# Performance work log

Hardware: AMD Instinct MI355X
Metric: run time of the kernel (lower is better)

## Reference

```python
import jax, jax.numpy as jnp
import numpy as np

EPS_BN = 1e-5


def _square_distance(a, b):
    # a: [B,N,3], b: [B,S,3] -> [B,N,S]
    return (jnp.sum(a * a, -1)[:, :, None]
            - 2.0 * jnp.einsum('bnc,bsc->bns', a, b)
            + jnp.sum(b * b, -1)[:, None, :])


def _bn_relu(x, gamma, beta):
    # x: [B,C,N]; training-mode batch norm over (B,N) per channel
    mean = jnp.mean(x, axis=(0, 2), keepdims=True)
    var = jnp.var(x, axis=(0, 2), keepdims=True)
    y = (x - mean) * jax.lax.rsqrt(var + EPS_BN)
    y = y * gamma[None, :, None] + beta[None, :, None]
    return jax.nn.relu(y)


def setup_inputs() -> dict:
    key = jax.random.key(0)
    ks = jax.random.split(key, 8)
    B, N, S, D1, D2 = 16, 4096, 1024, 128, 256
    Cin, C0, C1 = D1 + D2, 256, 128
    inp = {
        'xyz1': jax.random.normal(ks[0], (B, 3, N), jnp.float32),
        'xyz2': jax.random.normal(ks[1], (B, 3, S), jnp.float32),
        'points1': jax.random.normal(ks[2], (B, D1, N), jnp.float32),
        'points2': jax.random.normal(ks[3], (B, D2, S), jnp.float32),
        # pointwise Conv1d weights (kernel size 1) as [out,in]
        'w0': jax.random.normal(ks[4], (C0, Cin), jnp.float32) * (1.0 / np.sqrt(Cin)),
        'b0': jnp.zeros((C0,), jnp.float32),
        'g0': jnp.ones((C0,), jnp.float32),
        'be0': jnp.zeros((C0,), jnp.float32),
        'w1': jax.random.normal(ks[5], (C1, C0), jnp.float32) * (1.0 / np.sqrt(C0)),
        'b1': jnp.zeros((C1,), jnp.float32),
        'g1': jnp.ones((C1,), jnp.float32),
        'be1': jnp.zeros((C1,), jnp.float32),
    }
    return inp


def reference(xyz1, xyz2, points1, points2, w0, b0, g0, be0, w1, b1, g1, be1):
    # permute to [B,N,3] / [B,S,3] / [B,S,D2]
    x1 = jnp.transpose(xyz1, (0, 2, 1))
    x2 = jnp.transpose(xyz2, (0, 2, 1))
    p2 = jnp.transpose(points2, (0, 2, 1))
    B, N, _ = x1.shape

    dists = _square_distance(x1, x2)            # [B,N,S]
    # NOTE: faithful to the source: idx comes from the sort, but the
    # weight distances are the FIRST 3 columns of the UNsorted dists
    # (the repo assigns sorted values to `dicts`, not `dists`).
    idx = jnp.argsort(dists, axis=-1)[:, :, :3]  # [B,N,3]
    d3 = jnp.maximum(dists[:, :, :3], 1e-10)     # [B,N,3]
    weight = 1.0 / d3
    weight = weight / jnp.sum(weight, axis=-1, keepdims=True)

    gathered = jax.vmap(lambda p, i: p[i])(p2, idx)          # [B,N,3,D2]
    interpolated = jnp.sum(gathered * weight[..., None], axis=2)  # [B,N,D2]

    p1 = jnp.transpose(points1, (0, 2, 1))       # [B,N,D1]
    new_points = jnp.concatenate([p1, interpolated], axis=-1)  # [B,N,Cin]
    new_points = jnp.transpose(new_points, (0, 2, 1))           # [B,Cin,N]

    h = jnp.einsum('oc,bcn->bon', w0, new_points) + b0[None, :, None]
    h = _bn_relu(h, g0, be0)
    h = jnp.einsum('oc,bcn->bon', w1, h) + b1[None, :, None]
    h = _bn_relu(h, g1, be1)
    return h
```

## Files before the change

### kernel.cpp

```cpp
#include <hip/hip_runtime.h>
#include <cstdint>
#include <cstddef>

#define BB   16
#define NN   4096
#define SS   1024
#define D1   128
#define D2   256
#define CIN  384
#define C0   256
#define C1   128
#define MM   (BB*NN)
#define NBLK (MM/128)

typedef __attribute__((ext_vector_type(8))) short short8;
typedef __attribute__((ext_vector_type(4))) float f32x4;

__device__ __forceinline__ float b2f(unsigned short h) {
    union { unsigned int u; float f; } x; x.u = ((unsigned int)h) << 16; return x.f;
}
__device__ __forceinline__ unsigned short f2b(float f) {
    union { float f; unsigned int u; } x; x.f = f;
    unsigned int r = x.u + 0x7FFFu + ((x.u >> 16) & 1u);
    return (unsigned short)(r >> 16);
}

#define GLD16(g, l) __builtin_amdgcn_global_load_lds( \
    (const __attribute__((address_space(1))) void*)(g), \
    (__attribute__((address_space(3))) void*)(l), 16, 0, 0)

__global__ void transpose_cast_k(const float* __restrict__ src, unsigned short* __restrict__ dst,
                                 int C, int Np, int dstStride)
{
    __shared__ float tile[64][65];
    const int b = blockIdx.z, c0 = blockIdx.y * 64, n0 = blockIdx.x * 64;
    const int t = threadIdx.x, j = t & 63, i4 = t >> 6;
#pragma unroll
    for (int p = 0; p < 64; p += 4) {
        int ci = p + i4;
        tile[ci][j] = src[((size_t)b * C + c0 + ci) * Np + n0 + j];
    }
    __syncthreads();
#pragma unroll
    for (int p = 0; p < 64; p += 4) {
        int ni = p + i4;
        dst[((size_t)b * Np + n0 + ni) * dstStride + c0 + j] = f2b(tile[j][ni]);
    }
}

__global__ void cvtw_k(const float* __restrict__ w0, const float* __restrict__ w1,
                       unsigned short* __restrict__ w0b, unsigned short* __restrict__ w1b)
{
    int i = blockIdx.x * 256 + threadIdx.x;
    if (i < C0 * CIN) w0b[i] = f2b(w0[i]);
    if (i < C1 * C0)  w1b[i] = f2b(w1[i]);
}

#define UPD6(dd, ss, D0, D1v, D2v, J0, J1, J2) do { \
    bool ca = (dd) < D0, cb = (dd) < D1v, cc = (dd) < D2v; \
    float m1 = __builtin_amdgcn_fmed3f((dd), D0, D1v); \
    float m2 = __builtin_amdgcn_fmed3f((dd), D1v, D2v); \
    int u1 = ca ? J0 : (ss); \
    int u2 = cb ? J1 : (ss); \
    D0 = fminf((dd), D0); \
    J2 = cc ? u2 : J2; \
    J1 = cb ? u1 : J1; \
    J0 = ca ? (ss) : J0; \
    D1v = m1; D2v = m2; \
} while (0)

#define LTE(x, xj, y, yj) ((x) < (y) || ((x) == (y) && (xj) < (yj)))

__global__ __launch_bounds__(256) void knn_k(const float* __restrict__ xyz1,
                                             const float* __restrict__ xyz2,
                                             int* __restrict__ idxb, float* __restrict__ wtb)
{
    __shared__ __align__(16) float sx[8 * 132];
    __shared__ __align__(16) float sy[8 * 132];
    __shared__ __align__(16) float sz[8 * 132];
    const int b = blockIdx.y;
    const int t = threadIdx.x;
    const int chunk = t & 7;
    const int n = blockIdx.x * 32 + (t >> 3);

    for (int i = t; i < SS; i += 256) {
        int li = (i >> 7) * 132 + (i & 127);
        sx[li] = xyz2[((size_t)b * 3 + 0) * SS + i];
        sy[li] = xyz2[((size_t)b * 3 + 1) * SS + i];
        sz[li] = xyz2[((size_t)b * 3 + 2) * SS + i];
    }
    __syncthreads();

    const float px = xyz1[((size_t)b * 3 + 0) * NN + n];
    const float py = xyz1[((size_t)b * 3 + 1) * NN + n];
    const float pz = xyz1[((size_t)b * 3 + 2) * NN + n];

    float aD0 = 3.4e38f, aD1 = 3.4e38f, aD2 = 3.4e38f;
    int   aJ0 = 0, aJ1 = 0, aJ2 = 0;
    float bD0 = 3.4e38f, bD1 = 3.4e38f, bD2 = 3.4e38f;
    int   bJ0 = 0, bJ1 = 0, bJ2 = 0;

    const float* cx = sx + chunk * 132;
    const float* cy = sy + chunk * 132;
    const float* cz = sz + chunk * 132;
    const int sbase = chunk * 128;
#pragma unroll 4
    for (int s4 = 0; s4 < 32; ++s4) {
        float4 xs = *(const float4*)(cx + s4 * 4);
        float4 ys = *(const float4*)(cy + s4 * 4);
        float4 zs = *(const float4*)(cz + s4 * 4);
        int s = sbase + s4 * 4;
        { float dx=px-xs.x, dy=py-ys.x, dz=pz-zs.x; float d=dx*dx+dy*dy+dz*dz; UPD6(d, s+0, aD0,aD1,aD2,aJ0,aJ1,aJ2); }
        { float dx=px-xs.y, dy=py-ys.y, dz=pz-zs.y; float d=dx*dx+dy*dy+dz*dz; UPD6(d, s+1, bD0,bD1,bD2,bJ0,bJ1,bJ2); }
        { float dx=px-xs.z, dy=py-ys.z, dz=pz-zs.z; float d=dx*dx+dy*dy+dz*dz; UPD6(d, s+2, aD0,aD1,aD2,aJ0,aJ1,aJ2); }
        { float dx=px-xs.w, dy=py-ys.w, dz=pz-zs.w; float d=dx*dx+dy*dy+dz*dz; UPD6(d, s+3, bD0,bD1,bD2,bJ0,bJ1,bJ2); }
    }

    float d0v, d1v, d2v; int j0, j1, j2;
    {
        bool c0 = LTE(aD0, aJ0, bD0, bJ0);
        d0v = c0 ? aD0 : bD0;  j0 = c0 ? aJ0 : bJ0;
        float na0 = c0 ? aD1 : aD0, na1 = c0 ? aD2 : aD1;
        int   nx0 = c0 ? aJ1 : aJ0, nx1 = c0 ? aJ2 : aJ1;
        float nb0 = c0 ? bD0 : bD1, nb1 = c0 ? bD1 : bD2;
        int   ny0 = c0 ? bJ0 : bJ1, ny1 = c0 ? bJ1 : bJ2;
        bool c1 = LTE(na0, nx0, nb0, ny0);
        d1v = c1 ? na0 : nb0;  j1 = c1 ? nx0 : ny0;
        float ma0 = c1 ? na1 : na0;  int mx0 = c1 ? nx1 : nx0;
        float mb0 = c1 ? nb0 : nb1;  int my0 = c1 ? ny0 : ny1;
        bool c2 = LTE(ma0, mx0, mb0, my0);
        d2v = c2 ? ma0 : mb0;  j2 = c2 ? mx0 : my0;
    }

#pragma unroll
    for (int r = 1; r <= 4; r <<= 1) {
        float e0 = __shfl_xor(d0v, r), e1 = __shfl_xor(d1v, r), e2 = __shfl_xor(d2v, r);
        int   k0 = __shfl_xor(j0, r),  k1 = __shfl_xor(j1, r),  k2 = __shfl_xor(j2, r);
        bool ownlow = ((t & r) == 0);
        float a0 = ownlow ? d0v : e0, a1 = ownlow ? d1v : e1, a2 = ownlow ? d2v : e2;
        int   x0 = ownlow ? j0 : k0,  x1 = ownlow ? j1 : k1,  x2 = ownlow ? j2 : k2;
        float b0 = ownlow ? e0 : d0v, b1 = ownlow ? e1 : d1v, b2 = ownlow ? e2 : d2v;
        int   y0 = ownlow ? k0 : j0,  y1 = ownlow ? k1 : j1,  y2 = ownlow ? k2 : j2;
        bool c0 = a0 <= b0;
        d0v = c0 ? a0 : b0;  j0 = c0 ? x0 : y0;
        float na0 = c0 ? a1 : a0, na1 = c0 ? a2 : a1;
        int   nx0 = c0 ? x1 : x0, nx1 = c0 ? x2 : x1;
        float nb0 = c0 ? b0 : b1, nb1 = c0 ? b1 : b2;
        int   ny0 = c0 ? y0 : y1, ny1 = c0 ? y1 : y2;
        bool c1 = na0 <= nb0;
        d1v = c1 ? na0 : nb0;  j1 = c1 ? nx0 : ny0;
        float ma0 = c1 ? na1 : na0;  int mx0 = c1 ? nx1 : nx0;
        float mb0 = c1 ? nb0 : nb1;  int my0 = c1 ? ny0 : ny1;
        bool c2 = ma0 <= mb0;
        d2v = c2 ? ma0 : mb0;  j2 = c2 ? mx0 : my0;
    }

    if (chunk == 0) {
        float dd[3];
#pragma unroll
        for (int k = 0; k < 3; ++k) {
            float dx = px - sx[k], dy = py - sy[k], dz = pz - sz[k];
            float d = dx*dx + dy*dy + dz*dz;
            dd[k] = fmaxf(d, 1e-10f);
        }
        float r0 = 1.f/dd[0], r1 = 1.f/dd[1], r2 = 1.f/dd[2];
        float inv = 1.f / (r0 + r1 + r2);
        size_t base = ((size_t)b * NN + n) * 3;
        idxb[base+0] = j0; idxb[base+1] = j1; idxb[base+2] = j2;
        wtb[base+0] = r0*inv; wtb[base+1] = r1*inv; wtb[base+2] = r2*inv;
    }
}

__launch_bounds__(512, 1)
__global__ void gemm1_k(const unsigned short* __restrict__ P1T,
                        const unsigned short* __restrict__ P2T,
                        const int* __restrict__ idxb, const float* __restrict__ wtb,
                        const unsigned short* __restrict__ w0b,
                        unsigned short* __restrict__ h1, float* __restrict__ part1)
{
    __shared__ unsigned short Als[128 * 64];
    __shared__ unsigned short Bls[256 * 64];
    __shared__ float lsum[2][256];
    __shared__ float lsq[2][256];

    const int t = threadIdx.x;
    const int wv = t >> 6, l = t & 63, g = l >> 4, lc = l & 15;
    const int wm = wv >> 2, wn = wv & 3;
    const int m0 = blockIdx.x * 128;
    const int b  = blockIdx.x >> 5;
    const int sub = t & 7;

    const int grow = t >> 2;
    const size_t gb = ((size_t)(m0 + grow)) * 3;
    const int gi0 = idxb[gb], gi1 = idxb[gb+1], gi2 = idxb[gb+2];
    const float gw0 = wtb[gb], gw1 = wtb[gb+1], gw2 = wtb[gb+2];
    const char* gp0 = (const char*)(P2T + ((size_t)b * SS + gi0) * D2) + (t & 3) * 32;
    const char* gp1 = (const char*)(P2T + ((size_t)b * SS + gi1) * D2) + (t & 3) * 32;
    const char* gp2 = (const char*)(P2T + ((size_t)b * SS + gi2) * D2) + (t & 3) * 32;
    char* gdst = (char*)Als + grow * 128;
    const int gsw = (grow & 7) << 4;

    f32x4 acc[4][4];
#pragma unroll
    for (int i = 0; i < 4; ++i)
#pragma unroll
        for (int j = 0; j < 4; ++j) acc[i][j] = (f32x4){0.f, 0.f, 0.f, 0.f};

    for (int ks = 0; ks < 6; ++ks) {
        const int k0 = ks * 64;
        __syncthreads();
        if (ks < 2) {
#pragma unroll
            for (int q = 0; q < 2; ++q) {
                int row = q * 64 + (t >> 3);
                int bco = (sub * 16) ^ ((row & 7) << 4);
                const char* src = (const char*)P1T + (((size_t)(m0 + row)) * D1 + k0) * 2 + bco;
                char* dst = (char*)Als + (q * 512 + wv * 64) * 16;
                GLD16(src, dst);
            }
        } else {
            const int cgB = (ks - 2) * 128;
#pragma unroll
            for (int h = 0; h < 2; ++h) {
                union { uint4 v; unsigned short s[8]; } a0, a1, a2, ov;
                a0.v = *(const uint4*)(gp0 + cgB + h * 16);
                a1.v = *(const uint4*)(gp1 + cgB + h * 16);
                a2.v = *(const uint4*)(gp2 + cgB + h * 16);
#pragma unroll
                for (int i = 0; i < 8; ++i)
                    ov.s[i] = f2b(gw0 * b2f(a0.s[i]) + gw1 * b2f(a1.s[i]) + gw2 * b2f(a2.s[i]));
                *(uint4*)(gdst + (((t & 3) * 32 + h * 16) ^ gsw)) = ov.v;
            }
        }
#pragma unroll
        for (int q = 0; q < 4; ++q) {
            int o = q * 64 + (t >> 3);
            int bco = (sub * 16) ^ ((o & 7) << 4);
            const char* src = (const char*)w0b + (((size_t)o) * CIN + k0) * 2 + bco;
            char* dst = (char*)Bls + (q * 512 + wv * 64) * 16;
            GLD16(src, dst);
        }
        __syncthreads();
#pragma unroll
        for (int kk = 0; kk < 2; ++kk) {
            short8 af[4], bfr[4];
#pragma unroll
            for (int fm = 0; fm < 4; ++fm) {
                int row = wm * 64 + fm * 16 + lc;
                int bcol = kk * 64 + g * 16;
                af[fm] = *(const short8*)((const char*)Als + row * 128 + (bcol ^ ((row & 7) << 4)));
            }
#pragma unroll
            for (int fn = 0; fn < 4; ++fn) {
                int o = wn * 64 + fn * 16 + lc;
                int bcol = kk * 64 + g * 16;
                bfr[fn] = *(const short8*)((const char*)Bls + o * 128 + (bcol ^ ((o & 7) << 4)));
            }
#pragma unroll
            for (int fm = 0; fm < 4; ++fm)
#pragma unroll
                for (int fn = 0; fn < 4; ++fn)
                    acc[fm][fn] = __builtin_amdgcn_mfma_f32_16x16x32_bf16(af[fm], bfr[fn], acc[fm][fn], 0, 0, 0);
        }
    }

    float s1[4] = {0,0,0,0}, s2v[4] = {0,0,0,0};
#pragma unroll
    for (int fm = 0; fm < 4; ++fm)
#pragma unroll
        for (int fn = 0; fn < 4; ++fn) {
            int row = m0 + wm * 64 + fm * 16 + g * 4;
            int col = wn * 64 + fn * 16 + lc;
#pragma unroll
            for (int j = 0; j < 4; ++j) {
                float v = acc[fm][fn][j];
                h1[((size_t)(row + j)) * C0 + col] = f2b(v);
                s1[fn] += v; s2v[fn] += v * v;
            }
        }
#pragma unroll
    for (int fn = 0; fn < 4; ++fn) {
        s1[fn] += __shfl_xor(s1[fn], 16); s1[fn] += __shfl_xor(s1[fn], 32);
        s2v[fn] += __shfl_xor(s2v[fn], 16); s2v[fn] += __shfl_xor(s2v[fn], 32);
    }
    if (l < 16) {
#pragma unroll
        for (int fn = 0; fn < 4; ++fn) {
            lsum[wm][wn * 64 + fn * 16 + l] = s1[fn];
            lsq[wm][wn * 64 + fn * 16 + l] = s2v[fn];
        }
    }
    __syncthreads();
    if (t < 256) {
        part1[(size_t)t * NBLK + blockIdx.x]        = lsum[0][t] + lsum[1][t];
        part1[(size_t)(C0 + t) * NBLK + blockIdx.x] = lsq[0][t] + lsq[1][t];
    }
}

__global__ void stats_k(const float* __restrict__ part, int nblk, int C,
                        const float* __restrict__ gam, const float* __restrict__ bet,
                        float* __restrict__ sc, float* __restrict__ sh)
{
    const int w = threadIdx.x >> 6, l = threadIdx.x & 63;
    const int o = blockIdx.x * 4 + w;
    if (o >= C) return;
    float s = 0.f, q = 0.f;
    for (int i = l; i < nblk; i += 64) {
        s += part[(size_t)o * nblk + i];
        q += part[(size_t)(C + o) * nblk + i];
    }
#pragma unroll
    for (int r = 32; r; r >>= 1) { s += __shfl_xor(s, r); q += __shfl_xor(q, r); }
    if (l == 0) {
        const float inv = 1.0f / (float)MM;
        float mean = s * inv;
        float var = q * inv - mean * mean;
        float scale = gam[o] * rsqrtf(var + 1e-5f);
        sc[o] = scale;
        sh[o] = bet[o] - mean * scale;
    }
}

__launch_bounds__(256, 1)
__global__ void gemm2_k(const unsigned short* __restrict__ h1, const unsigned short* __restrict__ w1b,
                        const float* __restrict__ sc1, const float* __restrict__ sh1,
                        unsigned short* __restrict__ h2, float* __restrict__ part2)
{
    __shared__ unsigned short Als[128 * 64];
    __shared__ unsigned short Bls[128 * 64];
    __shared__ float scl[256], shl[256];
    __shared__ float lsum[2][128];
    __shared__ float lsq[2][128];

    const int t = threadIdx.x;
    const int wv = t >> 6, l = t & 63, g = l >> 4, lc = l & 15;
    const int wm = wv >> 1, wn = wv & 1;
    const int m0 = blockIdx.x * 128;
    const int sub = t & 7;

    scl[t] = sc1[t]; shl[t] = sh1[t];

    f32x4 acc[4][4];
#pragma unroll
    for (int i = 0; i < 4; ++i)
#pragma unroll
        for (int j = 0; j < 4; ++j) acc[i][j] = (f32x4){0.f, 0.f, 0.f, 0.f};

    for (int ks = 0; ks < 4; ++ks) {
        const int k0 = ks * 64;
        __syncthreads();
        uint4 r[4];
#pragma unroll
        for (int q = 0; q < 4; ++q) {
            int row = q * 32 + (t >> 3);
            r[q] = *(const uint4*)((const char*)h1 + (((size_t)(m0 + row)) * C0 + k0) * 2 + sub * 16);
        }
#pragma unroll
        for (int q = 0; q < 4; ++q) {
            int row = q * 32 + (t >> 3);
            union { uint4 v; unsigned short s[8]; } u, ov;
            u.v = r[q];
#pragma unroll
            for (int i = 0; i < 8; ++i) {
                int k = k0 + sub * 8 + i;
                float f = b2f(u.s[i]);
                ov.s[i] = f2b(fmaxf(0.0f, fmaf(scl[k], f, shl[k])));
            }
            *(uint4*)((char*)Als + row * 128 + ((sub * 16) ^ ((row & 7) << 4))) = ov.v;
        }
#pragma unroll
        for (int q = 0; q < 4; ++q) {
            int o = q * 32 + (t >> 3);
            int bco = (sub * 16) ^ ((o & 7) << 4);
            const char* src = (const char*)w1b + (((size_t)o) * C0 + k0) * 2 + bco;
            char* dst = (char*)Bls + (q * 256 + wv * 64) * 16;
            GLD16(src, dst);
        }
        __syncthreads();
#pragma unroll
        for (int kk = 0; kk < 2; ++kk) {
            short8 af[4], bfr[4];
#pragma unroll
            for (int fm = 0; fm < 4; ++fm) {
                int row = wm * 64 + fm * 16 + lc;
                int bcol = kk * 64 + g * 16;
                af[fm] = *(const short8*)((const char*)Als + row * 128 + (bcol ^ ((row & 7) << 4)));
            }
#pragma unroll
            for (int fn = 0; fn < 4; ++fn) {
                int o = wn * 64 + fn * 16 + lc;
                int bcol = kk * 64 + g * 16;
                bfr[fn] = *(const short8*)((const char*)Bls + o * 128 + (bcol ^ ((o & 7) << 4)));
            }
#pragma unroll
            for (int fm = 0; fm < 4; ++fm)
#pragma unroll
                for (int fn = 0; fn < 4; ++fn)
                    acc[fm][fn] = __builtin_amdgcn_mfma_f32_16x16x32_bf16(af[fm], bfr[fn], acc[fm][fn], 0, 0, 0);
        }
    }

    float s1[4] = {0,0,0,0}, s2v[4] = {0,0,0,0};
#pragma unroll
    for (int fm = 0; fm < 4; ++fm)
#pragma unroll
        for (int fn = 0; fn < 4; ++fn) {
            int row = m0 + wm * 64 + fm * 16 + g * 4;
            int col = wn * 64 + fn * 16 + lc;
#pragma unroll
            for (int j = 0; j < 4; ++j) {
                float v = acc[fm][fn][j];
                h2[((size_t)(row + j)) * C1 + col] = f2b(v);
                s1[fn] += v; s2v[fn] += v * v;
            }
        }
#pragma unroll
    for (int fn = 0; fn < 4; ++fn) {
        s1[fn] += __shfl_xor(s1[fn], 16); s1[fn] += __shfl_xor(s1[fn], 32);
        s2v[fn] += __shfl_xor(s2v[fn], 16); s2v[fn] += __shfl_xor(s2v[fn], 32);
    }
    if (l < 16) {
#pragma unroll
        for (int fn = 0; fn < 4; ++fn) {
            lsum[wm][wn * 64 + fn * 16 + l] = s1[fn];
            lsq[wm][wn * 64 + fn * 16 + l] = s2v[fn];
        }
    }
    __syncthreads();
    if (t < 128) {
        part2[(size_t)t * NBLK + blockIdx.x]        = lsum[0][t] + lsum[1][t];
        part2[(size_t)(C1 + t) * NBLK + blockIdx.x] = lsq[0][t] + lsq[1][t];
    }
}

__global__ void finalize_k(const unsigned short* __restrict__ h2,
                           const float* __restrict__ sc, const float* __restrict__ sh,
                           float* __restrict__ out)
{
    __shared__ float tile[64][65];
    const int b = blockIdx.z, o0 = blockIdx.y * 64, n0 = blockIdx.x * 64;
    const int t = threadIdx.x, j = t & 63, i4 = t >> 6;
    const float scv = sc[o0 + j], shv = sh[o0 + j];
#pragma unroll
    for (int p = 0; p < 64; p += 4) {
        int ni = p + i4;
        float f = b2f(h2[((size_t)b * NN + n0 + ni) * C1 + o0 + j]);
        tile[ni][j] = fmaxf(0.0f, fmaf(scv, f, shv));
    }
    __syncthreads();
#pragma unroll
    for (int p = 0; p < 64; p += 4) {
        int oi = p + i4;
        out[((size_t)(b * C1 + o0 + oi)) * NN + n0 + j] = tile[j][oi];
    }
}

extern "C" void kernel_launch(void* const* d_in, const int* in_sizes, int n_in,
                              void* d_out, int out_size, void* d_ws, size_t ws_size,
                              hipStream_t stream)
{
    const float* xyz1    = (const float*)d_in[0];
    const float* xyz2    = (const float*)d_in[1];
    const float* points1 = (const float*)d_in[2];
    const float* points2 = (const float*)d_in[3];
    const float* w0      = (const float*)d_in[4];
    const float* g0      = (const float*)d_in[6];
    const float* be0     = (const float*)d_in[7];
    const float* w1      = (const float*)d_in[8];
    const float* g1      = (const float*)d_in[10];
    const float* be1     = (const float*)d_in[11];
    float* out = (float*)d_out;
    char* ws = (char*)d_ws;

    unsigned short* P1T = (unsigned short*)(ws + 0);
    unsigned short* h1  = (unsigned short*)(ws + 16777216);
    unsigned short* P2T = (unsigned short*)(ws + 50331648);
    unsigned short* h2  = (unsigned short*)(ws + 58720256);
    int*   idxb  = (int*)  (ws + 75497472);
    float* wtb   = (float*)(ws + 76283904);
    unsigned short* w0b = (unsigned short*)(ws + 77070336);
    unsigned short* w1b = (unsigned short*)(ws + 77266944);
    float* part1 = (float*)(ws + 77332480);
    float* part2 = (float*)(ws + 78381056);
    float* sc1   = (float*)(ws + 78905344);
    float* sh1   = (float*)(ws + 78906368);
    float* sc2   = (float*)(ws + 78907392);
    float* sh2   = (float*)(ws + 78908416);

    transpose_cast_k<<<dim3(NN/64, D1/64, BB), 256, 0, stream>>>(points1, P1T, D1, NN, D1);
    transpose_cast_k<<<dim3(SS/64, D2/64, BB), 256, 0, stream>>>(points2, P2T, D2, SS, D2);
    cvtw_k<<<(C0*CIN)/256, 256, 0, stream>>>(w0, w1, w0b, w1b);
    knn_k<<<dim3(NN/32, BB), 256, 0, stream>>>(xyz1, xyz2, idxb, wtb);
    gemm1_k<<<MM/128, 512, 0, stream>>>(P1T, P2T, idxb, wtb, w0b, h1, part1);
    stats_k<<<C0/4, 256, 0, stream>>>(part1, NBLK, C0, g0, be0, sc1, sh1);
    gemm2_k<<<MM/128, 256, 0, stream>>>(h1, w1b, sc1, sh1, h2, part2);
    stats_k<<<C1/4, 256, 0, stream>>>(part2, NBLK, C1, g1, be1, sc2, sh2);
    finalize_k<<<dim3(NN/64, C1/64, BB), 256, 0, stream>>>(h2, sc2, sh2, out);
}
```

Measured before the change: 126.1 us.

## Fuse knn, transposes and weight casts into one interleaved front kernel

Replaces the four front-end launches (two transpose-casts, weight cast, knn) with one kernel whose blocks are interleaved by role, so each group of blocks mixes knn, transpose and cast work. This is meant to remove launch gaps and overlap the compute-bound knn search with the bandwidth-bound transposes. In exchange every block reserves the largest shared memory footprint, and the branches by block role add some divergence in scheduling.

Result: faster. 117.4 us (-6.9%).

```diff
diff --git a/kernel.cpp b/kernel.cpp
--- a/kernel.cpp
+++ b/kernel.cpp
@@ -29,32 +29,6 @@
     (const __attribute__((address_space(1))) void*)(g), \
     (__attribute__((address_space(3))) void*)(l), 16, 0, 0)
 
-__global__ void transpose_cast_k(const float* __restrict__ src, unsigned short* __restrict__ dst,
-                                 int C, int Np, int dstStride)
-{
-    __shared__ float tile[64][65];
-    const int b = blockIdx.z, c0 = blockIdx.y * 64, n0 = blockIdx.x * 64;
-    const int t = threadIdx.x, j = t & 63, i4 = t >> 6;
-#pragma unroll
-    for (int p = 0; p < 64; p += 4) {
-        int ci = p + i4;
-        tile[ci][j] = src[((size_t)b * C + c0 + ci) * Np + n0 + j];
-    }
-    __syncthreads();
-#pragma unroll
-    for (int p = 0; p < 64; p += 4) {
-        int ni = p + i4;
-        dst[((size_t)b * Np + n0 + ni) * dstStride + c0 + j] = f2b(tile[j][ni]);
-    }
-}
-
-__global__ void cvtw_k(const float* __restrict__ w0, const float* __restrict__ w1,
-                       unsigned short* __restrict__ w0b, unsigned short* __restrict__ w1b)
-{
-    int i = blockIdx.x * 256 + threadIdx.x;
-    if (i < C0 * CIN) w0b[i] = f2b(w0[i]);
-    if (i < C1 * C0)  w1b[i] = f2b(w1[i]);
-}
 
 #define UPD6(dd, ss, D0, D1v, D2v, J0, J1, J2) do { \
     bool ca = (dd) < D0, cb = (dd) < D1v, cc = (dd) < D2v; \
@@ -71,17 +45,18 @@
 
 #define LTE(x, xj, y, yj) ((x) < (y) || ((x) == (y) && (xj) < (yj)))
 
-__global__ __launch_bounds__(256) void knn_k(const float* __restrict__ xyz1,
-                                             const float* __restrict__ xyz2,
-                                             int* __restrict__ idxb, float* __restrict__ wtb)
-{
-    __shared__ __align__(16) float sx[8 * 132];
-    __shared__ __align__(16) float sy[8 * 132];
-    __shared__ __align__(16) float sz[8 * 132];
-    const int b = blockIdx.y;
-    const int t = threadIdx.x;
+__device__ __forceinline__ void knn_body(const float* __restrict__ xyz1,
+                                         const float* __restrict__ xyz2,
+                                         int* __restrict__ idxb, float* __restrict__ wtb,
+                                         int rb, int t, char* smem)
+{
+    float* sx = (float*)smem;
+    float* sy = sx + 8 * 132;
+    float* sz = sy + 8 * 132;
+    const int b = rb >> 7;
+    const int bx = rb & 127;
     const int chunk = t & 7;
-    const int n = blockIdx.x * 32 + (t >> 3);
+    const int n = bx * 32 + (t >> 3);
 
     for (int i = t; i < SS; i += 256) {
         int li = (i >> 7) * 132 + (i & 127);
@@ -171,6 +146,58 @@
     }
 }
 
+__device__ __forceinline__ void transpose_body(const float* __restrict__ src,
+                                               unsigned short* __restrict__ dst,
+                                               int C, int Np, int dstStride,
+                                               int b, int cblk, int nblk, int t, char* smem)
+{
+    float (*tile)[65] = (float(*)[65])smem;
+    const int c0 = cblk * 64, n0 = nblk * 64;
+    const int j = t & 63, i4 = t >> 6;
+#pragma unroll
+    for (int p = 0; p < 64; p += 4) {
+        int ci = p + i4;
+        tile[ci][j] = src[((size_t)b * C + c0 + ci) * Np + n0 + j];
+    }
+    __syncthreads();
+#pragma unroll
+    for (int p = 0; p < 64; p += 4) {
+        int ni = p + i4;
+        dst[((size_t)b * Np + n0 + ni) * dstStride + c0 + j] = f2b(tile[j][ni]);
+    }
+}
+
+__global__ __launch_bounds__(256) void mega_front_k(
+    const float* __restrict__ xyz1, const float* __restrict__ xyz2,
+    const float* __restrict__ points1, const float* __restrict__ points2,
+    const float* __restrict__ w0, const float* __restrict__ w1,
+    unsigned short* __restrict__ P1T, unsigned short* __restrict__ P2T,
+    unsigned short* __restrict__ w0b, unsigned short* __restrict__ w1b,
+    int* __restrict__ idxb, float* __restrict__ wtb)
+{
+    __shared__ __align__(16) char smem[16640];
+    const unsigned bid = blockIdx.x;
+    const int g = bid / 86, r = bid % 86;
+    const int t = threadIdx.x;
+
+    if (r < 32) {
+        knn_body(xyz1, xyz2, idxb, wtb, g * 32 + r, t, smem);
+    } else if (r < 64) {
+        int rb = g * 32 + (r - 32);
+        transpose_body(points1, P1T, D1, NN, D1,
+                       rb >> 7, (rb >> 6) & 1, rb & 63, t, smem);
+    } else if (r < 80) {
+        int rb = g * 16 + (r - 64);
+        transpose_body(points2, P2T, D2, SS, D2,
+                       rb >> 6, (rb >> 4) & 3, rb & 15, t, smem);
+    } else {
+        int rb = g * 6 + (r - 80);
+        int i = rb * 256 + t;
+        if (i < C0 * CIN) w0b[i] = f2b(w0[i]);
+        if (i < C1 * C0)  w1b[i] = f2b(w1[i]);
+    }
+}
+
 __launch_bounds__(512, 1)
 __global__ void gemm1_k(const unsigned short* __restrict__ P1T,
                         const unsigned short* __restrict__ P2T,
@@ -487,10 +514,8 @@
     float* sc2   = (float*)(ws + 78907392);
     float* sh2   = (float*)(ws + 78908416);
 
-    transpose_cast_k<<<dim3(NN/64, D1/64, BB), 256, 0, stream>>>(points1, P1T, D1, NN, D1);
-    transpose_cast_k<<<dim3(SS/64, D2/64, BB), 256, 0, stream>>>(points2, P2T, D2, SS, D2);
-    cvtw_k<<<(C0*CIN)/256, 256, 0, stream>>>(w0, w1, w0b, w1b);
-    knn_k<<<dim3(NN/32, BB), 256, 0, stream>>>(xyz1, xyz2, idxb, wtb);
+    mega_front_k<<<86 * 64, 256, 0, stream>>>(xyz1, xyz2, points1, points2, w0, w1,
+                                              P1T, P2T, w0b, w1b, idxb, wtb);
     gemm1_k<<<MM/128, 512, 0, stream>>>(P1T, P2T, idxb, wtb, w0b, h1, part1);
     stats_k<<<C0/4, 256, 0, stream>>>(part1, NBLK, C0, g0, be0, sc1, sh1);
     gemm2_k<<<MM/128, 256, 0, stream>>>(h1, w1b, sc1, sh1, h2, part2);
```
